# Performance work log

Measured on AMD Instinct MI355X. Metric: run time of the kernel, lower is better.

The kernel has to match this reference:

```python
import jax, jax.numpy as jnp
import numpy as np

B, N, E, H = 4, 2048, 288, 8
D = E // H  # head_dim = 36


def setup_inputs() -> dict:
    key = jax.random.key(0)
    ks = jax.random.split(key, 8)
    s = 1.0 / np.sqrt(E)
    return {
        "query": jax.random.normal(ks[0], (B, N, E), jnp.float32),
        "key": jax.random.normal(ks[1], (B, N, E), jnp.float32),
        "value": jax.random.normal(ks[2], (B, N, E), jnp.float32),
        "Wq": jax.random.normal(ks[3], (E, E), jnp.float32) * s,
        "bq": jnp.zeros((E,), jnp.float32),
        "Wk": jax.random.normal(ks[4], (E, E), jnp.float32) * s,
        "bk": jnp.zeros((E,), jnp.float32),
        "Wv": jax.random.normal(ks[5], (E, E), jnp.float32) * s,
        "bv": jnp.zeros((E,), jnp.float32),
        "Wo": jax.random.normal(ks[6], (E, E), jnp.float32) * s,
        "bo": jnp.zeros((E,), jnp.float32),
    }


def reference(query, key, value, Wq, bq, Wk, bk, Wv, bv, Wo, bo):
    scaling = float(D) ** (-0.5)
    q = (query @ Wq + bq) * scaling            # (B, N, E), pre-scaled as in source
    k = key @ Wk + bk                          # (B, N, E)
    v = value @ Wv + bv                        # (B, N, E)
    # split heads: per-head slices along last dim == reshape to (B, N, H, D)
    qh = q.reshape(B, N, H, D)
    kh = k.reshape(B, N, H, D)
    vh = v.reshape(B, N, H, D)
    scores = jnp.einsum("bnhd,bmhd->bhnm", qh, kh)   # (B, H, N, N)
    attn = jax.nn.softmax(scores, axis=-1)
    out = jnp.einsum("bhnm,bmhd->bnhd", attn, vh)    # (B, N, H, D)
    out = out.reshape(B, N, E)                       # concat heads
    return out @ Wo + bo
```

## Files before the change

kernel.cpp:

```cpp
#include <hip/hip_runtime.h>

#define E 288
#define NSEQ 2048
#define BATCH 4
#define NH 8
#define HD 36
#define BH (BATCH * NH)
#define ROWS (BATCH * NSEQ)
#define BHN (BH * NSEQ)

typedef _Float16 half8_t __attribute__((ext_vector_type(8)));
typedef _Float16 half4_t __attribute__((ext_vector_type(4)));
typedef _Float16 half2_t __attribute__((ext_vector_type(2)));
typedef float f32x4 __attribute__((ext_vector_type(4)));
typedef int i32x4 __attribute__((ext_vector_type(4)));

__device__ __forceinline__ int sw64(int row, int col) {
  return (row << 6) + ((((col >> 3) ^ row) & 7) << 3) + (col & 7);
}

__device__ __forceinline__ int toff(int r, int k) {
  const int rp = r >> 1;
  const int g = (((r & 1) << 2) + (k >> 3)) ^ (rp & 7);
  return (rp << 6) + ((g & 7) << 3) + (k & 7);
}

__device__ __forceinline__ void gld16(const _Float16* g, _Float16* l) {
  __builtin_amdgcn_global_load_lds(
      (const __attribute__((address_space(1))) void*)g,
      (__attribute__((address_space(3))) void*)l, 16, 0, 0);
}

__device__ __forceinline__ float fexp2(float x) {
  return __builtin_amdgcn_exp2f(x);
}

__device__ __forceinline__ unsigned pack_h2(float a, float b) {
  union { half2_t h; unsigned u; } cv;
  cv.h[0] = (_Float16)a;
  cv.h[1] = (_Float16)b;
  return cv.u;
}

__device__ __forceinline__ void plswap16(unsigned& a, unsigned& b) {
  asm("v_permlane16_swap_b32 %0, %1" : "+v"(a), "+v"(b));
}
__device__ __forceinline__ void plswap32(unsigned& a, unsigned& b) {
  asm("v_permlane32_swap_b32 %0, %1" : "+v"(a), "+v"(b));
}

#define WBLK 1296
#define QZBLK 1024
#define VOBLK 256

__global__ __launch_bounds__(256) void prep_kernel(
    const float* __restrict__ Wq, const float* __restrict__ Wk,
    const float* __restrict__ Wv, const float* __restrict__ Wo,
    _Float16* __restrict__ wblk, _Float16* __restrict__ q16,
    _Float16* __restrict__ vblk) {
  const int bid = blockIdx.x;
  const int tid = threadIdx.x;
  if (bid < WBLK) {
    const int j = bid * 256 + tid;
    const int m = j / (E * E);
    const int rem = j - m * (E * E);
    const int k = rem / E, n = rem - k * E;
    const float* W = (m == 0) ? Wq : (m == 1) ? Wk : (m == 2) ? Wv : Wo;
    wblk[(size_t)((m * 3 + n / 96) * 9 + (k >> 5)) * 3072 +
         toff(n % 96, k & 31)] = (_Float16)W[(size_t)k * E + n];
  } else if (bid < WBLK + QZBLK) {
    const int j = (bid - WBLK) * 256 + tid;
    const int row = j >> 2, sub = j & 3;
    ((i32x4*)q16)[(size_t)row * 8 + 4 + sub] = (i32x4){0, 0, 0, 0};
  } else {
    const int j = (bid - WBLK - QZBLK) * 256 + tid;
    const int bh = j >> 11;
    const int rem = j & 2047;
    const int kt = rem >> 6, c = rem & 63;
    vblk[((size_t)bh * 32 + kt) * 3072 + sw64(36, c)] = (_Float16)1.0f;
  }
}

#define PM 128
#define PN 96

struct QKVArgs {
  const float* x[3];
  const float* bias[3];
  _Float16* out[3];
};

__global__ __launch_bounds__(256, 4) void proj_qkv_kernel(
    QKVArgs A, const _Float16* __restrict__ wblk) {
  __shared__ __align__(16) _Float16 abuf[2][4096];
  __shared__ __align__(16) _Float16 wbuf[2][3072];

  const int tid = threadIdx.x;
  const int lane = tid & 63, w = tid >> 6;
  const int quad = lane >> 4, l15 = lane & 15;
  const int mode = blockIdx.z;
  const int RB = blockIdx.x, CT = blockIdx.y;
  const float* __restrict__ x = A.x[mode];
  const _Float16* __restrict__ wb = wblk + (size_t)(mode * 3 + CT) * 9 * 3072;
  const int row0 = RB * PM;

  float4 apre[4];
  auto loadA = [&](int C) {
#pragma unroll
    for (int iu = 0; iu < 4; ++iu) {
      const int i = tid + 256 * iu, r = i >> 3, c4 = i & 7;
      apre[iu] = *(const float4*)&x[(size_t)(row0 + r) * E + C * 32 + c4 * 4];
    }
  };
  auto writeA = [&](_Float16* dst) {
#pragma unroll
    for (int iu = 0; iu < 4; ++iu) {
      const int i = tid + 256 * iu, r = i >> 3, c4 = i & 7;
      half4_t h = {(_Float16)apre[iu].x, (_Float16)apre[iu].y,
                   (_Float16)apre[iu].z, (_Float16)apre[iu].w};
      *(half4_t*)&dst[toff(r, c4 * 4)] = h;
    }
  };

  f32x4 acc[2][6];
#pragma unroll
  for (int t = 0; t < 2; ++t)
#pragma unroll
    for (int nt = 0; nt < 6; ++nt) acc[t][nt] = (f32x4){0.f, 0.f, 0.f, 0.f};

  loadA(0);
  writeA(abuf[0]);
  for (int seg = w; seg < 6; seg += 4)
    gld16(wb + seg * 512 + lane * 8, wbuf[0] + seg * 512);
  loadA(1);

  for (int C = 0; C < 9; ++C) {
    const int cur = C & 1;
    __syncthreads();
    if (C + 1 < 9) {
      for (int seg = w; seg < 6; seg += 4)
        gld16(wb + (C + 1) * 3072 + seg * 512 + lane * 8,
              wbuf[cur ^ 1] + seg * 512);
      writeA(abuf[cur ^ 1]);
      if (C + 2 < 9) loadA(C + 2);
    }
    half8_t ah[2];
#pragma unroll
    for (int t = 0; t < 2; ++t)
      ah[t] = *(const half8_t*)&abuf[cur][toff(w * 32 + t * 16 + l15, quad * 8)];
#pragma unroll
    for (int nt = 0; nt < 6; ++nt) {
      const half8_t bf = *(const half8_t*)&wbuf[cur][toff(nt * 16 + l15, quad * 8)];
#pragma unroll
      for (int t = 0; t < 2; ++t)
        acc[t][nt] = __builtin_amdgcn_mfma_f32_16x16x32_f16(ah[t], bf, acc[t][nt], 0, 0, 0);
    }
  }

  const float* __restrict__ bias = A.bias[mode];
  _Float16* __restrict__ outp = A.out[mode];
  const float scale = (mode == 0) ? 0.24044917348149868f : 1.0f;
  const int col0 = CT * PN;
#pragma unroll
  for (int nt = 0; nt < 6; ++nt) {
    const int col = col0 + nt * 16 + l15;
    const int h = col / 36, d = col - h * 36;
    const float bc = bias[col];
#pragma unroll
    for (int t = 0; t < 2; ++t) {
#pragma unroll
      for (int r = 0; r < 4; ++r) {
        const int row = row0 + w * 32 + t * 16 + quad * 4 + r;
        const int b = row >> 11, n = row & (NSEQ - 1);
        const int bh = b * NH + h;
        const _Float16 val = (_Float16)((acc[t][nt][r] + bc) * scale);
        if (mode == 0) {
          outp[((size_t)bh * NSEQ + n) * 64 + d] = val;
        } else {
          const int kt = n >> 6, c = n & 63;
          if (mode == 1) {
            outp[((size_t)bh * 32 + kt) * 4096 + sw64(c, d)] = val;
          } else {
            const int pc = ((c & 15) << 2) | (c >> 4);
            outp[((size_t)bh * 32 + kt) * 3072 + sw64(d, pc)] = val;
          }
        }
      }
    }
  }
}

#define QB 128
#define KT 64
#define SPLIT 2
#define NIT (32 / SPLIT)

__device__ __forceinline__ void stage_tile(const _Float16* kg, const _Float16* vg,
                                           _Float16* kb, _Float16* vb, int w,
                                           int lane) {
#pragma unroll
  for (int seg = w; seg < 8; seg += 4)
    gld16(kg + seg * 512 + lane * 8, kb + seg * 512);
  for (int seg = w; seg < 6; seg += 4)
    gld16(vg + seg * 512 + lane * 8, vb + seg * 512);
}

__global__ __launch_bounds__(256, 4) void attn_kernel(
    const _Float16* __restrict__ q16, const _Float16* __restrict__ kblk,
    const _Float16* __restrict__ vblk, _Float16* __restrict__ pacc16,
    float* __restrict__ psum_r) {
  __shared__ __align__(16) _Float16 kbuf[2][KT * 64];
  __shared__ __align__(16) _Float16 vbuf[2][48 * 64];

  const int tid = threadIdx.x;
  const int lane = tid & 63;
  const int w = tid >> 6;
  const int quad = lane >> 4;
  const int l15 = lane & 15;

  const int id = blockIdx.x;
  const int xcd = id & 7;
  const int qb = (id >> 3) & 15;
  const int g = id >> 7;
  const int bhc = g * 8 + xcd;
  const int bh = bhc >> 1;
  const int chunk = bhc & 1;
  const int q0 = qb * QB;

  const _Float16* qbase = q16 + ((size_t)bh * NSEQ + q0 + w * 32) * 64;
  half8_t qf[2][2];
#pragma unroll
  for (int t = 0; t < 2; ++t)
#pragma unroll
    for (int kc = 0; kc < 2; ++kc)
      qf[t][kc] = *(const half8_t*)&qbase[(t * 16 + l15) * 64 + kc * 32 + quad * 8];

  f32x4 oacc[2][3];
#pragma unroll
  for (int t = 0; t < 2; ++t)
#pragma unroll
    for (int nt = 0; nt < 3; ++nt) oacc[t][nt] = (f32x4){0.f, 0.f, 0.f, 0.f};

  const f32x4 zf = (f32x4){0.f, 0.f, 0.f, 0.f};

  const int t0 = chunk * NIT;
  const _Float16* kbase = kblk + ((size_t)bh * 32 + t0) * 4096;
  const _Float16* vbase = vblk + ((size_t)bh * 32 + t0) * 3072;

  stage_tile(kbase, vbase, kbuf[0], vbuf[0], w, lane);

  for (int it = 0; it < NIT; ++it) {
    const int cur = it & 1;
    __syncthreads();
    if (it + 1 < NIT)
      stage_tile(kbase + (it + 1) * 4096, vbase + (it + 1) * 3072,
                 kbuf[cur ^ 1], vbuf[cur ^ 1], w, lane);

    half8_t vf[2][3];
#pragma unroll
    for (int kc = 0; kc < 2; ++kc)
#pragma unroll
      for (int nt = 0; nt < 3; ++nt)
        vf[kc][nt] = *(const half8_t*)&vbuf[cur][sw64(nt * 16 + l15, kc * 32 + quad * 8)];

    unsigned pk[2][4][2];
#pragma unroll
    for (int a = 0; a < 2; ++a) {
      f32x4 sc[2][2];
      __builtin_amdgcn_s_setprio(1);
#pragma unroll
      for (int sp = 0; sp < 2; ++sp) {
        const int s = a * 2 + sp;
        const half8_t kf0 = *(const half8_t*)&kbuf[cur][sw64(s * 16 + l15, quad * 8)];
        const half8_t kf1 = *(const half8_t*)&kbuf[cur][sw64(s * 16 + l15, 32 + quad * 8)];
#pragma unroll
        for (int t = 0; t < 2; ++t) {
          f32x4 c0 = __builtin_amdgcn_mfma_f32_16x16x32_f16(
              kf0, qf[t][0], zf, 0, 0, 0);
          sc[t][sp] = __builtin_amdgcn_mfma_f32_16x16x32_f16(
              kf1, qf[t][1], c0, 0, 0, 0);
        }
      }
      __builtin_amdgcn_s_setprio(0);
#pragma unroll
      for (int t = 0; t < 2; ++t)
#pragma unroll
        for (int r = 0; r < 4; ++r) {
          const float p0 = fexp2(sc[t][0][r]);
          const float p1 = fexp2(sc[t][1][r]);
          pk[t][r][a] = pack_h2(p0, p1);
        }
    }

    half8_t pa[2][2];
#pragma unroll
    for (int t = 0; t < 2; ++t) {
      union { unsigned u[4]; half8_t h; } f0, f1;
#pragma unroll
      for (int v = 0; v < 4; ++v) {
        unsigned x = pk[t][v >> 1][v & 1];
        unsigned y = pk[t][(v >> 1) + 2][v & 1];
        plswap16(x, y);
        plswap32(x, y);
        f0.u[v] = x;
        f1.u[v] = y;
      }
      pa[t][0] = f0.h;
      pa[t][1] = f1.h;
    }

    __builtin_amdgcn_s_setprio(1);
#pragma unroll
    for (int kc = 0; kc < 2; ++kc)
#pragma unroll
      for (int nt = 0; nt < 3; ++nt) {
#pragma unroll
        for (int t = 0; t < 2; ++t)
          oacc[t][nt] = __builtin_amdgcn_mfma_f32_16x16x32_f16(pa[t][kc], vf[kc][nt], oacc[t][nt], 0, 0, 0);
      }
    __builtin_amdgcn_s_setprio(0);
  }

  const int b = bh >> 3, h = bh & 7;
#pragma unroll
  for (int t = 0; t < 2; ++t) {
#pragma unroll
    for (int r = 0; r < 4; ++r) {
      const int n = q0 + w * 32 + t * 16 + quad * 4 + r;
      const size_t rowg = (size_t)b * NSEQ + n;
      const size_t base = ((size_t)chunk * ROWS + rowg) * E + h * 36;
      if (l15 == 4) psum_r[((size_t)chunk * ROWS + rowg) * 8 + h] = oacc[t][2][r];
#pragma unroll
      for (int nt = 0; nt < 3; ++nt) {
        const int col = nt * 16 + l15;
        if (col < HD) pacc16[base + col] = (_Float16)oacc[t][nt][r];
      }
    }
  }
}

__global__ __launch_bounds__(256, 4) void proj_o_kernel(
    const _Float16* __restrict__ pacc16, const float* __restrict__ psum_r,
    const _Float16* __restrict__ wblk_o, const float* __restrict__ bias,
    float* __restrict__ out) {
  __shared__ __align__(16) _Float16 hbuf[2][2048];
  __shared__ __align__(16) _Float16 lbuf[2][2048];
  __shared__ __align__(16) _Float16 wbuf[2][1536];
  __shared__ float invt[512];

  const int tid = threadIdx.x;
  const int lane = tid & 63, w = tid >> 6;
  const int quad = lane >> 4, l15 = lane & 15;
  const int RB = blockIdx.x, CT = blockIdx.y;
  const int row0 = RB * 64;
  const _Float16* __restrict__ wb =
      wblk_o + (size_t)(CT >> 1) * 9 * 3072 + (CT & 1) * 1536;

#pragma unroll
  for (int u = 0; u < 2; ++u) {
    const int idx = tid + u * 256;
    const int r = idx >> 3, hh = idx & 7;
    const float s = psum_r[(size_t)(row0 + r) * 8 + hh] +
                    psum_r[((size_t)ROWS + row0 + r) * 8 + hh];
    invt[idx] = 1.0f / s;
  }

  const int arow = tid >> 2;
  const int acol8 = (tid & 3) * 8;
  half8_t ap0, ap1;
  auto loadA = [&](int C) {
    const size_t off = (size_t)(row0 + arow) * E + C * 32 + acol8;
    ap0 = *(const half8_t*)&pacc16[off];
    ap1 = *(const half8_t*)&pacc16[(size_t)ROWS * E + off];
  };
  auto writeA = [&](int C, _Float16* hd, _Float16* ld) {
    const int colb = C * 32 + acol8;
    const int h0 = colb / 36;
    const int h1 = (colb + 7) / 36;
    const float i0 = invt[(arow << 3) + h0];
    const float i1 = invt[(arow << 3) + h1];
    const int split = h1 * 36 - colb;
    half8_t hv, lv;
#pragma unroll
    for (int j = 0; j < 8; ++j) {
      const float inv = (j < split) ? i0 : i1;
      const float a = (float)ap0[j] + (float)ap1[j];
      const float val = a * inv;
      const _Float16 hi = (_Float16)val;
      hv[j] = hi;
      lv[j] = (_Float16)(val - (float)hi);
    }
    *(half8_t*)&hd[toff(arow, acol8)] = hv;
    *(half8_t*)&ld[toff(arow, acol8)] = lv;
  };

  f32x4 acc[3];
#pragma unroll
  for (int nt = 0; nt < 3; ++nt) acc[nt] = (f32x4){0.f, 0.f, 0.f, 0.f};

  loadA(0);
  __syncthreads();
  writeA(0, hbuf[0], lbuf[0]);
  for (int seg = w; seg < 3; seg += 4)
    gld16(wb + seg * 512 + lane * 8, wbuf[0] + seg * 512);
  loadA(1);

  for (int C = 0; C < 9; ++C) {
    const int cur = C & 1;
    __syncthreads();
    if (C + 1 < 9) {
      for (int seg = w; seg < 3; seg += 4)
        gld16(wb + (C + 1) * 3072 + seg * 512 + lane * 8,
              wbuf[cur ^ 1] + seg * 512);
      writeA(C + 1, hbuf[cur ^ 1], lbuf[cur ^ 1]);
      if (C + 2 < 9) loadA(C + 2);
    }
    const half8_t ah = *(const half8_t*)&hbuf[cur][toff(w * 16 + l15, quad * 8)];
    const half8_t al = *(const half8_t*)&lbuf[cur][toff(w * 16 + l15, quad * 8)];
#pragma unroll
    for (int nt = 0; nt < 3; ++nt) {
      const half8_t bf = *(const half8_t*)&wbuf[cur][toff(nt * 16 + l15, quad * 8)];
      acc[nt] = __builtin_amdgcn_mfma_f32_16x16x32_f16(ah, bf, acc[nt], 0, 0, 0);
      acc[nt] = __builtin_amdgcn_mfma_f32_16x16x32_f16(al, bf, acc[nt], 0, 0, 0);
    }
  }

#pragma unroll
  for (int nt = 0; nt < 3; ++nt) {
    const int col = CT * 48 + nt * 16 + l15;
    const float bc = bias[col];
#pragma unroll
    for (int r = 0; r < 4; ++r) {
      const int row = row0 + w * 16 + quad * 4 + r;
      out[(size_t)row * E + col] = acc[nt][r] + bc;
    }
  }
}

extern "C" void kernel_launch(void* const* d_in, const int* in_sizes, int n_in,
                              void* d_out, int out_size, void* d_ws,
                              size_t ws_size, hipStream_t stream) {
  const float* query = (const float*)d_in[0];
  const float* key_ = (const float*)d_in[1];
  const float* value = (const float*)d_in[2];
  const float* Wq = (const float*)d_in[3];
  const float* bq = (const float*)d_in[4];
  const float* Wk = (const float*)d_in[5];
  const float* bk = (const float*)d_in[6];
  const float* Wv = (const float*)d_in[7];
  const float* bv = (const float*)d_in[8];
  const float* Wo = (const float*)d_in[9];
  const float* bo = (const float*)d_in[10];
  float* out = (float*)d_out;

  _Float16* q16 = (_Float16*)d_ws;
  _Float16* kblk = q16 + (size_t)BH * NSEQ * 64;
  _Float16* vblk = kblk + (size_t)BH * 32 * 4096;
  _Float16* wblk = vblk + (size_t)BH * 32 * 3072;
  _Float16* pacc16 = wblk + (size_t)4 * 3 * 9 * 3072;
  float* psum_r = (float*)(pacc16 + (size_t)SPLIT * ROWS * E);

  prep_kernel<<<WBLK + QZBLK + VOBLK, 256, 0, stream>>>(Wq, Wk, Wv, Wo, wblk,
                                                        q16, vblk);

  QKVArgs qa;
  qa.x[0] = query; qa.x[1] = key_; qa.x[2] = value;
  qa.bias[0] = bq; qa.bias[1] = bk; qa.bias[2] = bv;
  qa.out[0] = q16; qa.out[1] = kblk; qa.out[2] = vblk;
  proj_qkv_kernel<<<dim3(ROWS / PM, E / PN, 3), 256, 0, stream>>>(qa, wblk);

  attn_kernel<<<dim3((NSEQ / QB) * BH * SPLIT), 256, 0, stream>>>(
      q16, kblk, vblk, pacc16, psum_r);

  proj_o_kernel<<<dim3(ROWS / 64, E / 48), 256, 0, stream>>>(
      pacc16, psum_r, wblk + (size_t)3 * 3 * 9 * 3072, bo, out);
}
```

Before: 157.1 us.

## Pre-convert QKV activations to fp16 tiled blocks in prep kernel

The prep kernel gains an extra pass that converts query/key/value fp32 activations into fp16, swizzled 128x32 tile blocks in workspace. The QKV projection then stages the A tiles with direct global-to-LDS 16-byte loads instead of loading fp32 into registers, converting and writing LDS itself. It also stops re-reading fp32 activations once per column tile (three tiles per row block). The cost is an extra full pass that reads the fp32 inputs and writes an fp16 copy, plus more workspace memory.

Result: slower. 163.6 us (+4.1%).

```diff
diff --git a/kernel.cpp b/kernel.cpp
--- a/kernel.cpp
+++ b/kernel.cpp
@@ -52,12 +52,15 @@
 #define WBLK 1296
 #define QZBLK 1024
 #define VOBLK 256
+#define XBLK 3456
 
 __global__ __launch_bounds__(256) void prep_kernel(
     const float* __restrict__ Wq, const float* __restrict__ Wk,
     const float* __restrict__ Wv, const float* __restrict__ Wo,
-    _Float16* __restrict__ wblk, _Float16* __restrict__ q16,
-    _Float16* __restrict__ vblk) {
+    const float* __restrict__ xq, const float* __restrict__ xk,
+    const float* __restrict__ xv, _Float16* __restrict__ wblk,
+    _Float16* __restrict__ q16, _Float16* __restrict__ vblk,
+    _Float16* __restrict__ xblk) {
   const int bid = blockIdx.x;
   const int tid = threadIdx.x;
   if (bid < WBLK) {
@@ -72,26 +75,39 @@
     const int j = (bid - WBLK) * 256 + tid;
     const int row = j >> 2, sub = j & 3;
     ((i32x4*)q16)[(size_t)row * 8 + 4 + sub] = (i32x4){0, 0, 0, 0};
-  } else {
+  } else if (bid < WBLK + QZBLK + VOBLK) {
     const int j = (bid - WBLK - QZBLK) * 256 + tid;
     const int bh = j >> 11;
     const int rem = j & 2047;
     const int kt = rem >> 6, c = rem & 63;
     vblk[((size_t)bh * 32 + kt) * 3072 + sw64(36, c)] = (_Float16)1.0f;
+  } else {
+    const int j = (bid - WBLK - QZBLK - VOBLK) * 256 + tid;
+    const int m = j / (ROWS * 36);
+    const int rem = j - m * (ROWS * 36);
+    const int row = rem / 36, c8 = rem - row * 36;
+    const int col = c8 * 8;
+    const float* x = (m == 0) ? xq : (m == 1) ? xk : xv;
+    const float4 a = *(const float4*)&x[(size_t)row * E + col];
+    const float4 b = *(const float4*)&x[(size_t)row * E + col + 4];
+    half8_t h = {(_Float16)a.x, (_Float16)a.y, (_Float16)a.z, (_Float16)a.w,
+                 (_Float16)b.x, (_Float16)b.y, (_Float16)b.z, (_Float16)b.w};
+    *(half8_t*)&xblk[(size_t)((m * 64 + (row >> 7)) * 9 + (col >> 5)) * 4096 +
+                     toff(row & 127, col & 31)] = h;
   }
 }
 
 #define PM 128
 #define PN 96
 
-struct QKVArgs {
-  const float* x[3];
+struct QKVOut {
   const float* bias[3];
   _Float16* out[3];
 };
 
 __global__ __launch_bounds__(256, 4) void proj_qkv_kernel(
-    QKVArgs A, const _Float16* __restrict__ wblk) {
+    QKVOut A, const _Float16* __restrict__ wblk,
+    const _Float16* __restrict__ xblk) {
   __shared__ __align__(16) _Float16 abuf[2][4096];
   __shared__ __align__(16) _Float16 wbuf[2][3072];
 
@@ -100,26 +116,18 @@
   const int quad = lane >> 4, l15 = lane & 15;
   const int mode = blockIdx.z;
   const int RB = blockIdx.x, CT = blockIdx.y;
-  const float* __restrict__ x = A.x[mode];
   const _Float16* __restrict__ wb = wblk + (size_t)(mode * 3 + CT) * 9 * 3072;
+  const _Float16* __restrict__ xb = xblk + (size_t)(mode * 64 + RB) * 9 * 4096;
   const int row0 = RB * PM;
 
-  float4 apre[4];
-  auto loadA = [&](int C) {
-#pragma unroll
-    for (int iu = 0; iu < 4; ++iu) {
-      const int i = tid + 256 * iu, r = i >> 3, c4 = i & 7;
-      apre[iu] = *(const float4*)&x[(size_t)(row0 + r) * E + C * 32 + c4 * 4];
-    }
+  auto stageA = [&](int C, _Float16* dst) {
+#pragma unroll
+    for (int seg = w; seg < 8; seg += 4)
+      gld16(xb + C * 4096 + seg * 512 + lane * 8, dst + seg * 512);
   };
-  auto writeA = [&](_Float16* dst) {
-#pragma unroll
-    for (int iu = 0; iu < 4; ++iu) {
-      const int i = tid + 256 * iu, r = i >> 3, c4 = i & 7;
-      half4_t h = {(_Float16)apre[iu].x, (_Float16)apre[iu].y,
-                   (_Float16)apre[iu].z, (_Float16)apre[iu].w};
-      *(half4_t*)&dst[toff(r, c4 * 4)] = h;
-    }
+  auto stageW = [&](int C, _Float16* dst) {
+    for (int seg = w; seg < 6; seg += 4)
+      gld16(wb + C * 3072 + seg * 512 + lane * 8, dst + seg * 512);
   };
 
   f32x4 acc[2][6];
@@ -128,21 +136,15 @@
 #pragma unroll
     for (int nt = 0; nt < 6; ++nt) acc[t][nt] = (f32x4){0.f, 0.f, 0.f, 0.f};
 
-  loadA(0);
-  writeA(abuf[0]);
-  for (int seg = w; seg < 6; seg += 4)
-    gld16(wb + seg * 512 + lane * 8, wbuf[0] + seg * 512);
-  loadA(1);
+  stageA(0, abuf[0]);
+  stageW(0, wbuf[0]);
 
   for (int C = 0; C < 9; ++C) {
     const int cur = C & 1;
     __syncthreads();
     if (C + 1 < 9) {
-      for (int seg = w; seg < 6; seg += 4)
-        gld16(wb + (C + 1) * 3072 + seg * 512 + lane * 8,
-              wbuf[cur ^ 1] + seg * 512);
-      writeA(abuf[cur ^ 1]);
-      if (C + 2 < 9) loadA(C + 2);
+      stageW(C + 1, wbuf[cur ^ 1]);
+      stageA(C + 1, abuf[cur ^ 1]);
     }
     half8_t ah[2];
 #pragma unroll
@@ -457,17 +459,18 @@
   _Float16* kblk = q16 + (size_t)BH * NSEQ * 64;
   _Float16* vblk = kblk + (size_t)BH * 32 * 4096;
   _Float16* wblk = vblk + (size_t)BH * 32 * 3072;
-  _Float16* pacc16 = wblk + (size_t)4 * 3 * 9 * 3072;
+  _Float16* xblk = wblk + (size_t)4 * 3 * 9 * 3072;
+  _Float16* pacc16 = xblk + (size_t)3 * 64 * 9 * 4096;
   float* psum_r = (float*)(pacc16 + (size_t)SPLIT * ROWS * E);
 
-  prep_kernel<<<WBLK + QZBLK + VOBLK, 256, 0, stream>>>(Wq, Wk, Wv, Wo, wblk,
-                                                        q16, vblk);
-
-  QKVArgs qa;
-  qa.x[0] = query; qa.x[1] = key_; qa.x[2] = value;
+  prep_kernel<<<WBLK + QZBLK + VOBLK + XBLK, 256, 0, stream>>>(
+      Wq, Wk, Wv, Wo, query, key_, value, wblk, q16, vblk, xblk);
+
+  QKVOut qa;
   qa.bias[0] = bq; qa.bias[1] = bk; qa.bias[2] = bv;
   qa.out[0] = q16; qa.out[1] = kblk; qa.out[2] = vblk;
-  proj_qkv_kernel<<<dim3(ROWS / PM, E / PN, 3), 256, 0, stream>>>(qa, wblk);
+  proj_qkv_kernel<<<dim3(ROWS / PM, E / PN, 3), 256, 0, stream>>>(qa, wblk,
+                                                                  xblk);
 
   attn_kernel<<<dim3((NSEQ / QB) * BH * SPLIT), 256, 0, stream>>>(
       q16, kblk, vblk, pacc16, psum_r);
```
